# Optimization experiments

Hardware: AMD Instinct MI355X
Metric: run time of the kernel (lower is better)

Reference implementation:

```python
import jax, jax.numpy as jnp
import numpy as np

B, K, L, D = 16, 64, 128, 768  # batch, top_k, max_length, embedding_dim


def setup_inputs() -> dict:
    key = jax.random.key(0)
    context = jax.random.normal(key, (B, K, 2, L, D), dtype=jnp.float32)
    return {"context": context}


def reference(context):
    # context: [B, K, 2, L, D]; slot 0 = mention context tokens, slot 1 = entity tokens
    ctx = context[:, :, 0]  # [B, K, L, D]
    ent = context[:, :, 1]  # [B, K, L, D]
    # token-token similarity per (batch, candidate): [B, K, L, L]
    sim = jnp.einsum("bkld,bkmd->bklm", ctx, ent)
    # per-context-token best entity token (hard argmax, non-differentiable index)
    idx = jnp.argmax(sim, axis=-1)  # [B, K, L] int
    # gather matched entity vectors: [B, K, L, D]
    ent_matched = jnp.take_along_axis(ent, idx[..., None], axis=2)
    # dot product per token then sum over tokens -> sum-of-max score [B, K]
    out = jnp.sum(ctx * ent_matched, axis=(-2, -1))
    return out
```

## Files before the change

### kernel.cpp

```cpp
#include <hip/hip_runtime.h>


typedef __attribute__((ext_vector_type(8))) __bf16 bf16x8;
typedef __attribute__((ext_vector_type(4))) __bf16 bf16x4;
typedef __attribute__((ext_vector_type(4))) float f32x4;

#define L_DIM 128
#define D_DIM 768
#define DC    64
#define LDP   72

__global__ __launch_bounds__(256, 4)
void som_kernel(const float* __restrict__ context, float* __restrict__ out) {
    const int bk   = blockIdx.x;
    const int t    = threadIdx.x;
    const int lane = t & 63;
    const int wave = t >> 6;
    const int quad = (lane >> 4) & 3;
    const int l15  = lane & 15;

    const float* ctx_g = context + (size_t)bk * (2 * L_DIM * D_DIM);
    const float* ent_g = ctx_g + (size_t)(L_DIM * D_DIM);

    __shared__ __bf16 ctx_s[L_DIM * LDP];
    __shared__ __bf16 ent_s[L_DIM * LDP];
    __shared__ float wave_sum[4];

    f32x4 acc[2][8];
    const f32x4 zero = {0.f, 0.f, 0.f, 0.f};
#pragma unroll
    for (int rt = 0; rt < 2; ++rt)
#pragma unroll
        for (int ct = 0; ct < 8; ++ct)
            acc[rt][ct] = zero;

    for (int c = 0; c < D_DIM / DC; ++c) {
        __syncthreads();
#pragma unroll 2
        for (int i = 0; i < 8; ++i) {
            const int g   = t + i * 256;
            const int row = g >> 4;
            const int c4  = g & 15;
            const int goff = row * D_DIM + c * DC + c4 * 4;
            const float4 vc = *(const float4*)(ctx_g + goff);
            const float4 ve = *(const float4*)(ent_g + goff);
            bf16x4 pc = {(__bf16)vc.x, (__bf16)vc.y, (__bf16)vc.z, (__bf16)vc.w};
            bf16x4 pe = {(__bf16)ve.x, (__bf16)ve.y, (__bf16)ve.z, (__bf16)ve.w};
            *(bf16x4*)&ctx_s[row * LDP + c4 * 4] = pc;
            *(bf16x4*)&ent_s[row * LDP + c4 * 4] = pe;
        }
        __syncthreads();

#pragma unroll
        for (int ks = 0; ks < 2; ++ks) {
            const bf16x8 a0 = *(const bf16x8*)&ctx_s[(wave * 32 + l15) * LDP + ks * 32 + quad * 8];
            const bf16x8 a1 = *(const bf16x8*)&ctx_s[(wave * 32 + 16 + l15) * LDP + ks * 32 + quad * 8];
#pragma unroll
            for (int ct = 0; ct < 8; ++ct) {
                const bf16x8 b = *(const bf16x8*)&ent_s[(ct * 16 + l15) * LDP + ks * 32 + quad * 8];
                acc[0][ct] = __builtin_amdgcn_mfma_f32_16x16x32_bf16(a0, b, acc[0][ct], 0, 0, 0);
                acc[1][ct] = __builtin_amdgcn_mfma_f32_16x16x32_bf16(a1, b, acc[1][ct], 0, 0, 0);
            }
        }
    }

    float total = 0.f;
#pragma unroll
    for (int rt = 0; rt < 2; ++rt) {
#pragma unroll
        for (int reg = 0; reg < 4; ++reg) {
            float m = acc[rt][0][reg];
#pragma unroll
            for (int ct = 1; ct < 8; ++ct) m = fmaxf(m, acc[rt][ct][reg]);
            m = fmaxf(m, __shfl_xor(m, 1, 64));
            m = fmaxf(m, __shfl_xor(m, 2, 64));
            m = fmaxf(m, __shfl_xor(m, 4, 64));
            m = fmaxf(m, __shfl_xor(m, 8, 64));
            total += m;
        }
    }
    total += __shfl_xor(total, 16, 64);
    total += __shfl_xor(total, 32, 64);

    if (lane == 0) wave_sum[wave] = total;
    __syncthreads();
    if (t == 0)
        out[bk] = wave_sum[0] + wave_sum[1] + wave_sum[2] + wave_sum[3];
}

extern "C" void kernel_launch(void* const* d_in, const int* in_sizes, int n_in,
                              void* d_out, int out_size, void* d_ws, size_t ws_size,
                              hipStream_t stream) {
    const float* context = (const float*)d_in[0];
    float* out = (float*)d_out;
    som_kernel<<<dim3(1024), dim3(256), 0, stream>>>(context, out);
}
```

Before: 996.7 us.

## Double-buffer LDS tiles with register prefetch to overlap loads with MFMA

Replaces the load-sync-compute loop with a double-buffered LDS pipeline. The next D-chunk is prefetched into registers before the MFMAs on the current buffer, then converted and written to the other buffer afterwards, which removes one barrier per iteration. The chunk size drops from 64 to 32 so the two buffers fit, which doubles the number of iterations. Launch bounds move from 4 to 3 blocks per SM to allow the extra registers, at the cost of occupancy.

```diff
diff --git a/kernel.cpp b/kernel.cpp
--- a/kernel.cpp
+++ b/kernel.cpp
@@ -7,10 +7,11 @@
 
 #define L_DIM 128
 #define D_DIM 768
-#define DC    64
-#define LDP   72
+#define DC    32
+#define NCH   (D_DIM / DC)
+#define LDP   40
 
-__global__ __launch_bounds__(256, 4)
+__global__ __launch_bounds__(256, 3)
 void som_kernel(const float* __restrict__ context, float* __restrict__ out) {
     const int bk   = blockIdx.x;
     const int t    = threadIdx.x;
@@ -20,10 +21,9 @@
     const int l15  = lane & 15;
 
     const float* ctx_g = context + (size_t)bk * (2 * L_DIM * D_DIM);
-    const float* ent_g = ctx_g + (size_t)(L_DIM * D_DIM);
 
-    __shared__ __bf16 ctx_s[L_DIM * LDP];
-    __shared__ __bf16 ent_s[L_DIM * LDP];
+    __shared__ __bf16 ctx_s[2][L_DIM * LDP];
+    __shared__ __bf16 ent_s[2][L_DIM * LDP];
     __shared__ float wave_sum[4];
 
     f32x4 acc[2][8];
@@ -34,34 +34,48 @@
         for (int ct = 0; ct < 8; ++ct)
             acc[rt][ct] = zero;
 
-    for (int c = 0; c < D_DIM / DC; ++c) {
+    const int row0 = t >> 3;
+    const int c4   = t & 7;
+    const float* gbase = ctx_g + (size_t)row0 * D_DIM + c4 * 4;
+
+    float4 pc[4], pe[4];
+
+    auto load_regs = [&](int c) {
+#pragma unroll
+        for (int i = 0; i < 4; ++i) {
+            const float* p = gbase + (size_t)i * 32 * D_DIM + c * DC;
+            pc[i] = *(const float4*)p;
+            pe[i] = *(const float4*)(p + L_DIM * D_DIM);
+        }
+    };
+    auto cvt_write = [&](int b) {
+#pragma unroll
+        for (int i = 0; i < 4; ++i) {
+            bf16x4 qc = {(__bf16)pc[i].x, (__bf16)pc[i].y, (__bf16)pc[i].z, (__bf16)pc[i].w};
+            bf16x4 qe = {(__bf16)pe[i].x, (__bf16)pe[i].y, (__bf16)pe[i].z, (__bf16)pe[i].w};
+            *(bf16x4*)&ctx_s[b][(row0 + i * 32) * LDP + c4 * 4] = qc;
+            *(bf16x4*)&ent_s[b][(row0 + i * 32) * LDP + c4 * 4] = qe;
+        }
+    };
+
+    load_regs(0);
+    cvt_write(0);
+
+    int p = 0;
+    for (int c = 0; c < NCH; ++c, p ^= 1) {
         __syncthreads();
-#pragma unroll 2
-        for (int i = 0; i < 8; ++i) {
-            const int g   = t + i * 256;
-            const int row = g >> 4;
-            const int c4  = g & 15;
-            const int goff = row * D_DIM + c * DC + c4 * 4;
-            const float4 vc = *(const float4*)(ctx_g + goff);
-            const float4 ve = *(const float4*)(ent_g + goff);
-            bf16x4 pc = {(__bf16)vc.x, (__bf16)vc.y, (__bf16)vc.z, (__bf16)vc.w};
-            bf16x4 pe = {(__bf16)ve.x, (__bf16)ve.y, (__bf16)ve.z, (__bf16)ve.w};
-            *(bf16x4*)&ctx_s[row * LDP + c4 * 4] = pc;
-            *(bf16x4*)&ent_s[row * LDP + c4 * 4] = pe;
+        if (c + 1 < NCH) load_regs(c + 1);
+
+        const bf16x8 a0 = *(const bf16x8*)&ctx_s[p][(wave * 32 + l15) * LDP + quad * 8];
+        const bf16x8 a1 = *(const bf16x8*)&ctx_s[p][(wave * 32 + 16 + l15) * LDP + quad * 8];
+#pragma unroll
+        for (int ct = 0; ct < 8; ++ct) {
+            const bf16x8 b = *(const bf16x8*)&ent_s[p][(ct * 16 + l15) * LDP + quad * 8];
+            acc[0][ct] = __builtin_amdgcn_mfma_f32_16x16x32_bf16(a0, b, acc[0][ct], 0, 0, 0);
+            acc[1][ct] = __builtin_amdgcn_mfma_f32_16x16x32_bf16(a1, b, acc[1][ct], 0, 0, 0);
         }
-        __syncthreads();
 
-#pragma unroll
-        for (int ks = 0; ks < 2; ++ks) {
-            const bf16x8 a0 = *(const bf16x8*)&ctx_s[(wave * 32 + l15) * LDP + ks * 32 + quad * 8];
-            const bf16x8 a1 = *(const bf16x8*)&ctx_s[(wave * 32 + 16 + l15) * LDP + ks * 32 + quad * 8];
-#pragma unroll
-            for (int ct = 0; ct < 8; ++ct) {
-                const bf16x8 b = *(const bf16x8*)&ent_s[(ct * 16 + l15) * LDP + ks * 32 + quad * 8];
-                acc[0][ct] = __builtin_amdgcn_mfma_f32_16x16x32_bf16(a0, b, acc[0][ct], 0, 0, 0);
-                acc[1][ct] = __builtin_amdgcn_mfma_f32_16x16x32_bf16(a1, b, acc[1][ct], 0, 0, 0);
-            }
-        }
+        if (c + 1 < NCH) cvt_write(p ^ 1);
     }
 
     float total = 0.f;
```

Measured after the change: 1.005 ms. No clear change (+0.8%).
